# Kernel tuning notes

Hardware: AMD Instinct MI355X
Metric: run time of the kernel (lower is better)

Reference implementation:

```python
import jax, jax.numpy as jnp
import numpy as np

WINDOW_SIZE = 3
STRIDE = 3
CHANNEL = 3
SIGMA = 1.5
C1 = 0.01 ** 2
C2 = 0.03 ** 2


def _make_window():
    # 1D gaussian (sigma=1.5), normalized, outer product -> 2D window, tiled per channel [C,1,ws,ws]
    ws = WINDOW_SIZE
    g = np.exp(-((np.arange(ws) - ws // 2) ** 2) / (2.0 * SIGMA ** 2))
    g = (g / g.sum()).astype(np.float32)
    w2 = np.outer(g, g)
    return jnp.asarray(np.tile(w2[None, None], (CHANNEL, 1, 1, 1)))


def _dwconv(x, w):
    # depthwise conv2d, padding=(ws-1)//2, stride=STRIDE, groups=CHANNEL
    pad = (WINDOW_SIZE - 1) // 2
    return jax.lax.conv_general_dilated(
        x, w,
        window_strides=(STRIDE, STRIDE),
        padding=[(pad, pad), (pad, pad)],
        dimension_numbers=("NCHW", "OIHW", "NCHW"),
        feature_group_count=CHANNEL,
    )


def setup_inputs() -> dict:
    key = jax.random.key(0)
    k1, k2 = jax.random.split(key)
    img1 = jax.random.uniform(k1, (16, 3, 512, 512), dtype=jnp.float32)
    img2 = jax.random.uniform(k2, (16, 3, 512, 512), dtype=jnp.float32)
    return {"img1": img1, "img2": img2, "window": _make_window()}


def reference(img1, img2, window):
    mu1 = _dwconv(img1, window)
    mu2 = _dwconv(img2, window)
    mu1_sq = mu1 * mu1
    mu2_sq = mu2 * mu2
    mu1_mu2 = mu1 * mu2
    sigma1_sq = _dwconv(img1 * img1, window) - mu1_sq
    sigma2_sq = _dwconv(img2 * img2, window) - mu2_sq
    sigma12 = _dwconv(img1 * img2, window) - mu1_mu2
    ssim_map = (2.0 * mu1_mu2 + C1) * (2.0 * sigma12 + C2) / (
        (mu1_sq + mu2_sq + C1) * (sigma1_sq + sigma2_sq + C2)
    )
    # size_average=True -> scalar mean
    return ssim_map.mean()
```

## Files before the change

### kernel.cpp

```cpp
#include <hip/hip_runtime.h>


#define HW       512
#define PLANE_SZ (HW * HW)
#define OHW      171
#define NPLANE   48
#define NOUT     (NPLANE * OHW * OHW)
#define NTASK    (NPLANE * OHW)
#define TPB      256
#define WPB      4
#define NBLK     (NTASK / WPB)

typedef float f4 __attribute__((ext_vector_type(4)));

__device__ __forceinline__ float ssim_val(float s1, float s2, float s11,
                                          float s22, float s12) {
  const float C1 = 1e-4f, C2 = 9e-4f;
  const float m11 = s1 * s1, m22 = s2 * s2, m12 = s1 * s2;
  const float sg1 = s11 - m11, sg2 = s22 - m22, sg12 = s12 - m12;
  return ((2.0f * m12 + C1) * (2.0f * sg12 + C2)) /
         ((m11 + m22 + C1) * (sg1 + sg2 + C2));
}

__global__ __launch_bounds__(TPB) void ssim_main(
    const float* __restrict__ img1, const float* __restrict__ img2,
    const float* __restrict__ win, float* __restrict__ partial) {
  const int lane  = threadIdx.x & 63;
  const int wv    = threadIdx.x >> 6;
  const int task  = blockIdx.x * WPB + wv;
  const int plane = task / OHW;
  const int oy    = task - plane * OHW;

  float wy[3], wx[3];
#pragma unroll
  for (int k = 0; k < 3; ++k) {
    wy[k] = win[3 * k] + win[3 * k + 1] + win[3 * k + 2];
    wx[k] = win[k] + win[k + 3] + win[k + 6];
  }
  const int r0 = 3 * oy - 1;
  float wyv[3];
  wyv[0] = (r0 >= 0) ? wy[0] : 0.0f;
  wyv[1] = wy[1];
  wyv[2] = wy[2];
  const int rr0 = (r0 < 0) ? 0 : r0;

  const float* a = img1 + (size_t)plane * PLANE_SZ;
  const float* b = img2 + (size_t)plane * PLANE_SZ;

  f4 xa[3][2], xb[3][2];
#pragma unroll
  for (int k = 0; k < 3; ++k) {
    const int r = (k == 0) ? rr0 : (r0 + k);
    const f4* ra = (const f4*)(a + (size_t)r * HW);
    const f4* rb = (const f4*)(b + (size_t)r * HW);
    xa[k][0] = ra[lane];      xa[k][1] = ra[lane + 64];
    xb[k][0] = rb[lane];      xb[k][1] = rb[lane + 64];
  }

  float acc = 0.0f;
  float fwd[5];

#pragma unroll
  for (int c = 0; c < 2; ++c) {
    const int m = (lane + c) % 3;

    float P1[4]  = {0.f, 0.f, 0.f, 0.f};
    float P2[4]  = {0.f, 0.f, 0.f, 0.f};
    float P11[4] = {0.f, 0.f, 0.f, 0.f};
    float P22[4] = {0.f, 0.f, 0.f, 0.f};
    float P12[4] = {0.f, 0.f, 0.f, 0.f};
#pragma unroll
    for (int k = 0; k < 3; ++k) {
      const float wyk = wyv[k];
#pragma unroll
      for (int j = 0; j < 4; ++j) {
        const float x = xa[k][c][j];
        const float y = xb[k][c][j];
        const float u = wyk * x;
        const float v = wyk * y;
        P1[j] += u;
        P2[j] += v;
        P11[j] = fmaf(u, x, P11[j]);
        P22[j] = fmaf(v, y, P22[j]);
        P12[j] = fmaf(u, y, P12[j]);
      }
    }

    float wxl[4];
#pragma unroll
    for (int j = 0; j < 4; ++j) {
      const int ix = (m + j + 1) % 3;
      wxl[j] = (ix == 0) ? wx[0] : ((ix == 1) ? wx[1] : wx[2]);
    }

    const float aL = (m != 1) ? 1.0f : 0.0f;
    const float bL = (m == 2) ? 1.0f : 0.0f;
    float L[5], R[5];
    {
      float t0, t1, t2, t3, full, left;
#define BIN(Q, P)                                              \
      t0 = wxl[0] * P[0]; t1 = wxl[1] * P[1];                  \
      t2 = wxl[2] * P[2]; t3 = wxl[3] * P[3];                  \
      full = (t0 + t1) + (t2 + t3);                            \
      left = fmaf(bL, t2, fmaf(aL, t1, t0));                   \
      L[Q] = left; R[Q] = full - left;
      BIN(0, P1) BIN(1, P2) BIN(2, P11) BIN(3, P22) BIN(4, P12)
#undef BIN
    }
    if (c == 0) {
#pragma unroll
      for (int q = 0; q < 5; ++q) fwd[q] = R[q];
    }

    const float allow =
        (m != 2 && !(c == 0 && lane == 0)) ? 1.0f : 0.0f;
#pragma unroll
    for (int q = 0; q < 5; ++q) {
      float up = __shfl_up(R[q], 1, 64);
      if (c == 1) {
        const float seam = __shfl(fwd[q], 63, 64);
        up = (lane == 0) ? seam : up;
      }
      L[q] = fmaf(allow, up, L[q]);
    }

    const float mR = (m == 1) ? 1.0f : 0.0f;
    acc += ssim_val(L[0], L[1], L[2], L[3], L[4]);
    acc += mR * ssim_val(R[0], R[1], R[2], R[3], R[4]);
  }

#pragma unroll
  for (int off = 32; off > 0; off >>= 1) acc += __shfl_down(acc, off, 64);
  __shared__ float wsum[TPB / 64];
  if (lane == 0) wsum[wv] = acc;
  __syncthreads();
  if (threadIdx.x == 0) {
    float s = 0.f;
#pragma unroll
    for (int i = 0; i < TPB / 64; ++i) s += wsum[i];
    partial[blockIdx.x] = s;
  }
}

__global__ __launch_bounds__(256) void ssim_final(
    const float* __restrict__ partial, float* __restrict__ out) {
  double acc = 0.0;
  for (int i = threadIdx.x; i < NBLK; i += 256) acc += (double)partial[i];
#pragma unroll
  for (int off = 32; off > 0; off >>= 1) acc += __shfl_down(acc, off, 64);
  __shared__ double wsum[4];
  const int lane = threadIdx.x & 63, wid = threadIdx.x >> 6;
  if (lane == 0) wsum[wid] = acc;
  __syncthreads();
  if (threadIdx.x == 0) {
    double s = 0.0;
#pragma unroll
    for (int i = 0; i < 4; ++i) s += wsum[i];
    out[0] = (float)(s / (double)NOUT);
  }
}

extern "C" void kernel_launch(void* const* d_in, const int* in_sizes, int n_in,
                              void* d_out, int out_size, void* d_ws, size_t ws_size,
                              hipStream_t stream) {
  const float* img1 = (const float*)d_in[0];
  const float* img2 = (const float*)d_in[1];
  const float* win  = (const float*)d_in[2];
  float* partial = (float*)d_ws;
  float* out = (float*)d_out;

  ssim_main<<<NBLK, TPB, 0, stream>>>(img1, img2, win, partial);
  ssim_final<<<1, 256, 0, stream>>>(partial, out);
}
```

Measured before the change: 119.9 us.

## Split each output row across two wavefronts and use fast reciprocal

Each output row is now handled by two wavefronts, one per half of the input row, which doubles the number of wavefronts and halves the per-wave work and register load. The second half recomputes the seam contribution from the last float4 of the first half instead of passing it through a cross-lane shuffle. The SSIM division is replaced with a hardware reciprocal multiply. This trades a small redundant load and compute at the seam, and slightly lower reciprocal precision, for more parallelism and latency hiding on what is a bandwidth-bound kernel.

```diff
diff --git a/kernel.cpp b/kernel.cpp
--- a/kernel.cpp
+++ b/kernel.cpp
@@ -6,7 +6,7 @@
 #define OHW      171
 #define NPLANE   48
 #define NOUT     (NPLANE * OHW * OHW)
-#define NTASK    (NPLANE * OHW)
+#define NTASK    (NPLANE * OHW * 2)
 #define TPB      256
 #define WPB      4
 #define NBLK     (NTASK / WPB)
@@ -18,18 +18,21 @@
   const float C1 = 1e-4f, C2 = 9e-4f;
   const float m11 = s1 * s1, m22 = s2 * s2, m12 = s1 * s2;
   const float sg1 = s11 - m11, sg2 = s22 - m22, sg12 = s12 - m12;
-  return ((2.0f * m12 + C1) * (2.0f * sg12 + C2)) /
-         ((m11 + m22 + C1) * (sg1 + sg2 + C2));
+  const float num = (2.0f * m12 + C1) * (2.0f * sg12 + C2);
+  const float den = (m11 + m22 + C1) * (sg1 + sg2 + C2);
+  return num * __builtin_amdgcn_rcpf(den);
 }
 
 __global__ __launch_bounds__(TPB) void ssim_main(
     const float* __restrict__ img1, const float* __restrict__ img2,
     const float* __restrict__ win, float* __restrict__ partial) {
-  const int lane  = threadIdx.x & 63;
-  const int wv    = threadIdx.x >> 6;
-  const int task  = blockIdx.x * WPB + wv;
-  const int plane = task / OHW;
-  const int oy    = task - plane * OHW;
+  const int lane = threadIdx.x & 63;
+  const int wv   = threadIdx.x >> 6;
+  const int task = blockIdx.x * WPB + wv;
+  const int plane = task / (2 * OHW);
+  const int rem   = task - plane * (2 * OHW);
+  const int oy    = rem >> 1;
+  const int h     = rem & 1;
 
   float wy[3], wx[3];
 #pragma unroll
@@ -47,87 +50,112 @@
   const float* a = img1 + (size_t)plane * PLANE_SZ;
   const float* b = img2 + (size_t)plane * PLANE_SZ;
 
-  f4 xa[3][2], xb[3][2];
+  f4 xa[3], xb[3], pa[3], pb[3];
+  const f4* ra0;
 #pragma unroll
   for (int k = 0; k < 3; ++k) {
     const int r = (k == 0) ? rr0 : (r0 + k);
     const f4* ra = (const f4*)(a + (size_t)r * HW);
     const f4* rb = (const f4*)(b + (size_t)r * HW);
-    xa[k][0] = ra[lane];      xa[k][1] = ra[lane + 64];
-    xb[k][0] = rb[lane];      xb[k][1] = rb[lane + 64];
-  }
-
-  float acc = 0.0f;
-  float fwd[5];
-
-#pragma unroll
-  for (int c = 0; c < 2; ++c) {
-    const int m = (lane + c) % 3;
-
-    float P1[4]  = {0.f, 0.f, 0.f, 0.f};
-    float P2[4]  = {0.f, 0.f, 0.f, 0.f};
-    float P11[4] = {0.f, 0.f, 0.f, 0.f};
-    float P22[4] = {0.f, 0.f, 0.f, 0.f};
-    float P12[4] = {0.f, 0.f, 0.f, 0.f};
+    const int s = 64 * h + lane;
+    xa[k] = ra[s];
+    xb[k] = rb[s];
+    if (h) {
+      pa[k] = ra[63];
+      pb[k] = rb[63];
+    } else {
+      pa[k] = (f4){0.f, 0.f, 0.f, 0.f};
+      pb[k] = (f4){0.f, 0.f, 0.f, 0.f};
+    }
+    (void)ra0;
+  }
+
+  float P1[4] = {0,0,0,0}, P2[4] = {0,0,0,0}, P11[4] = {0,0,0,0},
+        P22[4] = {0,0,0,0}, P12[4] = {0,0,0,0};
+#pragma unroll
+  for (int k = 0; k < 3; ++k) {
+    const float wyk = wyv[k];
+#pragma unroll
+    for (int j = 0; j < 4; ++j) {
+      const float x = xa[k][j], y = xb[k][j];
+      const float u = wyk * x, v = wyk * y;
+      P1[j] += u;  P2[j] += v;
+      P11[j] = fmaf(u, x, P11[j]);
+      P22[j] = fmaf(v, y, P22[j]);
+      P12[j] = fmaf(u, y, P12[j]);
+    }
+  }
+
+  const int m = (h + lane) % 3;
+  float wxl[4];
+#pragma unroll
+  for (int j = 0; j < 4; ++j) {
+    const int ix = (m + j + 1) % 3;
+    wxl[j] = (ix == 0) ? wx[0] : ((ix == 1) ? wx[1] : wx[2]);
+  }
+  const float aL = (m != 1) ? 1.0f : 0.0f;
+  const float bL = (m == 2) ? 1.0f : 0.0f;
+
+  float L[5], R[5];
+  {
+    float t0, t1, t2, t3, full, left;
+#define BIN(Q, PP)                                             \
+    t0 = wxl[0] * PP[0]; t1 = wxl[1] * PP[1];                  \
+    t2 = wxl[2] * PP[2]; t3 = wxl[3] * PP[3];                  \
+    full = (t0 + t1) + (t2 + t3);                              \
+    left = fmaf(bL, t2, fmaf(aL, t1, t0));                     \
+    L[Q] = left; R[Q] = full - left;
+    BIN(0, P1) BIN(1, P2) BIN(2, P11) BIN(3, P22) BIN(4, P12)
+#undef BIN
+  }
+
+  float Rp[5] = {0.f, 0.f, 0.f, 0.f, 0.f};
+  if (h) {
+    float Q1[4] = {0,0,0,0}, Q2[4] = {0,0,0,0}, Q11[4] = {0,0,0,0},
+          Q22[4] = {0,0,0,0}, Q12[4] = {0,0,0,0};
 #pragma unroll
     for (int k = 0; k < 3; ++k) {
       const float wyk = wyv[k];
 #pragma unroll
       for (int j = 0; j < 4; ++j) {
-        const float x = xa[k][c][j];
-        const float y = xb[k][c][j];
-        const float u = wyk * x;
-        const float v = wyk * y;
-        P1[j] += u;
-        P2[j] += v;
-        P11[j] = fmaf(u, x, P11[j]);
-        P22[j] = fmaf(v, y, P22[j]);
-        P12[j] = fmaf(u, y, P12[j]);
+        const float x = pa[k][j], y = pb[k][j];
+        const float u = wyk * x, v = wyk * y;
+        Q1[j] += u;  Q2[j] += v;
+        Q11[j] = fmaf(u, x, Q11[j]);
+        Q22[j] = fmaf(v, y, Q22[j]);
+        Q12[j] = fmaf(u, y, Q12[j]);
       }
     }
-
-    float wxl[4];
+    const int mp = (h + 2) % 3;
+    float wxp[4];
 #pragma unroll
     for (int j = 0; j < 4; ++j) {
-      const int ix = (m + j + 1) % 3;
-      wxl[j] = (ix == 0) ? wx[0] : ((ix == 1) ? wx[1] : wx[2]);
-    }
-
-    const float aL = (m != 1) ? 1.0f : 0.0f;
-    const float bL = (m == 2) ? 1.0f : 0.0f;
-    float L[5], R[5];
-    {
-      float t0, t1, t2, t3, full, left;
-#define BIN(Q, P)                                              \
-      t0 = wxl[0] * P[0]; t1 = wxl[1] * P[1];                  \
-      t2 = wxl[2] * P[2]; t3 = wxl[3] * P[3];                  \
-      full = (t0 + t1) + (t2 + t3);                            \
-      left = fmaf(bL, t2, fmaf(aL, t1, t0));                   \
-      L[Q] = left; R[Q] = full - left;
-      BIN(0, P1) BIN(1, P2) BIN(2, P11) BIN(3, P22) BIN(4, P12)
-#undef BIN
-    }
-    if (c == 0) {
-#pragma unroll
-      for (int q = 0; q < 5; ++q) fwd[q] = R[q];
-    }
-
-    const float allow =
-        (m != 2 && !(c == 0 && lane == 0)) ? 1.0f : 0.0f;
-#pragma unroll
-    for (int q = 0; q < 5; ++q) {
-      float up = __shfl_up(R[q], 1, 64);
-      if (c == 1) {
-        const float seam = __shfl(fwd[q], 63, 64);
-        up = (lane == 0) ? seam : up;
-      }
-      L[q] = fmaf(allow, up, L[q]);
-    }
-
-    const float mR = (m == 1) ? 1.0f : 0.0f;
-    acc += ssim_val(L[0], L[1], L[2], L[3], L[4]);
-    acc += mR * ssim_val(R[0], R[1], R[2], R[3], R[4]);
-  }
+      const int ix = (mp + j + 1) % 3;
+      wxp[j] = (ix == 0) ? wx[0] : ((ix == 1) ? wx[1] : wx[2]);
+    }
+    const float aP = (mp != 1) ? 1.0f : 0.0f;
+    const float bP = (mp == 2) ? 1.0f : 0.0f;
+    float t0, t1, t2, t3, full, left;
+#define BINP(Q, PP)                                            \
+    t0 = wxp[0] * PP[0]; t1 = wxp[1] * PP[1];                  \
+    t2 = wxp[2] * PP[2]; t3 = wxp[3] * PP[3];                  \
+    full = (t0 + t1) + (t2 + t3);                              \
+    left = fmaf(bP, t2, fmaf(aP, t1, t0));                     \
+    Rp[Q] = full - left;
+    BINP(0, Q1) BINP(1, Q2) BINP(2, Q11) BINP(3, Q22) BINP(4, Q12)
+#undef BINP
+  }
+
+  const float allow = (m != 2) ? 1.0f : 0.0f;
+#pragma unroll
+  for (int q = 0; q < 5; ++q) {
+    float up = __shfl_up(R[q], 1, 64);
+    if (lane == 0) up = Rp[q];
+    L[q] = fmaf(allow, up, L[q]);
+  }
+
+  float acc = ssim_val(L[0], L[1], L[2], L[3], L[4]);
+  if (m == 1) acc += ssim_val(R[0], R[1], R[2], R[3], R[4]);
 
 #pragma unroll
   for (int off = 32; off > 0; off >>= 1) acc += __shfl_down(acc, off, 64);
```

Result: no change. 120.7 us (+0.6%).

## Process four row-tasks per wave with software-prefetched loads and fast reciprocal

Applied to the files above, without the earlier changes.

Each wave now handles four consecutive output rows, prefetching the next row's six-row input tile into registers while computing the current one, which aims to overlap global-memory latency with compute and cut block count and reduction overhead. The SSIM division is replaced with a hardware reciprocal times the numerator, trading exact division for a slightly less accurate approximation. Register pressure roughly doubles from the double-buffered tiles, and launch bounds now request a minimum occupancy of three blocks.

```diff
diff --git a/kernel.cpp b/kernel.cpp
--- a/kernel.cpp
+++ b/kernel.cpp
@@ -7,59 +7,55 @@
 #define NPLANE   48
 #define NOUT     (NPLANE * OHW * OHW)
 #define NTASK    (NPLANE * OHW)
+#define TPW      4
+#define NWAVE    (NTASK / TPW)
 #define TPB      256
 #define WPB      4
-#define NBLK     (NTASK / WPB)
+#define NBLK     (NWAVE / WPB)
 
 typedef float f4 __attribute__((ext_vector_type(4)));
+
+struct TD { f4 xa[3][2]; f4 xb[3][2]; };
 
 __device__ __forceinline__ float ssim_val(float s1, float s2, float s11,
                                           float s22, float s12) {
   const float C1 = 1e-4f, C2 = 9e-4f;
   const float m11 = s1 * s1, m22 = s2 * s2, m12 = s1 * s2;
   const float sg1 = s11 - m11, sg2 = s22 - m22, sg12 = s12 - m12;
-  return ((2.0f * m12 + C1) * (2.0f * sg12 + C2)) /
-         ((m11 + m22 + C1) * (sg1 + sg2 + C2));
-}
-
-__global__ __launch_bounds__(TPB) void ssim_main(
-    const float* __restrict__ img1, const float* __restrict__ img2,
-    const float* __restrict__ win, float* __restrict__ partial) {
-  const int lane  = threadIdx.x & 63;
-  const int wv    = threadIdx.x >> 6;
-  const int task  = blockIdx.x * WPB + wv;
+  const float num = (2.0f * m12 + C1) * (2.0f * sg12 + C2);
+  const float den = (m11 + m22 + C1) * (sg1 + sg2 + C2);
+  return num * __builtin_amdgcn_rcpf(den);
+}
+
+__device__ __forceinline__ void load_task(const float* __restrict__ img1,
+                                          const float* __restrict__ img2,
+                                          int task, int lane, TD& d) {
   const int plane = task / OHW;
   const int oy    = task - plane * OHW;
-
-  float wy[3], wx[3];
-#pragma unroll
-  for (int k = 0; k < 3; ++k) {
-    wy[k] = win[3 * k] + win[3 * k + 1] + win[3 * k + 2];
-    wx[k] = win[k] + win[k + 3] + win[k + 6];
-  }
-  const int r0 = 3 * oy - 1;
-  float wyv[3];
-  wyv[0] = (r0 >= 0) ? wy[0] : 0.0f;
-  wyv[1] = wy[1];
-  wyv[2] = wy[2];
-  const int rr0 = (r0 < 0) ? 0 : r0;
-
+  const int r0    = 3 * oy - 1;
+  const int rr0   = (r0 < 0) ? 0 : r0;
   const float* a = img1 + (size_t)plane * PLANE_SZ;
   const float* b = img2 + (size_t)plane * PLANE_SZ;
-
-  f4 xa[3][2], xb[3][2];
 #pragma unroll
   for (int k = 0; k < 3; ++k) {
     const int r = (k == 0) ? rr0 : (r0 + k);
     const f4* ra = (const f4*)(a + (size_t)r * HW);
     const f4* rb = (const f4*)(b + (size_t)r * HW);
-    xa[k][0] = ra[lane];      xa[k][1] = ra[lane + 64];
-    xb[k][0] = rb[lane];      xb[k][1] = rb[lane + 64];
-  }
+    d.xa[k][0] = ra[lane];      d.xa[k][1] = ra[lane + 64];
+    d.xb[k][0] = rb[lane];      d.xb[k][1] = rb[lane + 64];
+  }
+}
+
+__device__ __forceinline__ float task_ssim(const TD& d, int oy, int lane,
+                                           float wy0, float wy1, float wy2,
+                                           float wx0, float wx1, float wx2) {
+  float wyv[3];
+  wyv[0] = (oy == 0) ? 0.0f : wy0;
+  wyv[1] = wy1;
+  wyv[2] = wy2;
 
   float acc = 0.0f;
   float fwd[5];
-
 #pragma unroll
   for (int c = 0; c < 2; ++c) {
     const int m = (lane + c) % 3;
@@ -74,8 +70,8 @@
       const float wyk = wyv[k];
 #pragma unroll
       for (int j = 0; j < 4; ++j) {
-        const float x = xa[k][c][j];
-        const float y = xb[k][c][j];
+        const float x = d.xa[k][c][j];
+        const float y = d.xb[k][c][j];
         const float u = wyk * x;
         const float v = wyk * y;
         P1[j] += u;
@@ -90,7 +86,7 @@
 #pragma unroll
     for (int j = 0; j < 4; ++j) {
       const int ix = (m + j + 1) % 3;
-      wxl[j] = (ix == 0) ? wx[0] : ((ix == 1) ? wx[1] : wx[2]);
+      wxl[j] = (ix == 0) ? wx0 : ((ix == 1) ? wx1 : wx2);
     }
 
     const float aL = (m != 1) ? 1.0f : 0.0f;
@@ -128,6 +124,38 @@
     acc += ssim_val(L[0], L[1], L[2], L[3], L[4]);
     acc += mR * ssim_val(R[0], R[1], R[2], R[3], R[4]);
   }
+  return acc;
+}
+
+__global__ __launch_bounds__(TPB, 3) void ssim_main(
+    const float* __restrict__ img1, const float* __restrict__ img2,
+    const float* __restrict__ win, float* __restrict__ partial) {
+  const int lane = threadIdx.x & 63;
+  const int wv   = threadIdx.x >> 6;
+  const int wave = blockIdx.x * WPB + wv;
+  const int base = wave * TPW;
+
+  float wy[3], wx[3];
+#pragma unroll
+  for (int k = 0; k < 3; ++k) {
+    wy[k] = win[3 * k] + win[3 * k + 1] + win[3 * k + 2];
+    wx[k] = win[k] + win[k + 3] + win[k + 6];
+  }
+
+  TD cur, nxt;
+  load_task(img1, img2, base, lane, cur);
+
+  float acc = 0.0f;
+#pragma unroll
+  for (int t = 0; t < TPW; ++t) {
+    if (t + 1 < TPW)
+      load_task(img1, img2, base + t + 1, lane, nxt);
+    const int task  = base + t;
+    const int plane = task / OHW;
+    const int oy    = task - plane * OHW;
+    acc += task_ssim(cur, oy, lane, wy[0], wy[1], wy[2], wx[0], wx[1], wx[2]);
+    if (t + 1 < TPW) cur = nxt;
+  }
 
 #pragma unroll
   for (int off = 32; off > 0; off >>= 1) acc += __shfl_down(acc, off, 64);
```

Measured after the change: 119.4 us. Within noise of the previous version (-0.5%).
